# Kernel optimization log

Measured on AMD Instinct MI355X. Metric: run time of the kernel, lower is better.

## Reference

```python
import jax, jax.numpy as jnp
import numpy as np
from math import sqrt

D_K = 64
HEADS = 16


def setup_inputs() -> dict:
    key = jax.random.key(0)
    k1, k2, k3 = jax.random.split(key, 3)
    B, S, D = 2, 2048, HEADS * D_K
    queries = jax.random.normal(k1, (B, S, D), dtype=jnp.float32)
    keys = jax.random.normal(k2, (B, S, D), dtype=jnp.float32)
    values = jax.random.normal(k3, (B, S, D), dtype=jnp.float32)
    # causal mask: 1 where attention is disallowed (j > i), 0 elsewhere
    mask = jnp.triu(jnp.ones((S, S), dtype=jnp.int32), k=1)[None, None]  # [1,1,S,S]
    return {"queries": queries, "keys": keys, "values": values, "mask": mask}


def reference(queries, keys, values, mask):
    B, S, _ = queries.shape
    # [B, S, H*Dk] -> [B, H, S, Dk]
    def split_heads(x):
        return x.reshape(B, -1, HEADS, D_K).transpose(0, 2, 1, 3)

    q = split_heads(queries)
    k = split_heads(keys)
    v = split_heads(values)
    # scores: [B, H, Sq, Sk]
    attn = jnp.einsum('bhqd,bhkd->bhqk', q, k) / sqrt(D_K)
    attn = attn + mask.astype(attn.dtype) * jnp.asarray(-1e9, attn.dtype)
    w = jax.nn.softmax(attn, axis=-1)
    out = jnp.einsum('bhqk,bhkd->bhqd', w, v)  # [B, H, Sq, Dk]
    return out
```

## Files before the change

kernel.cpp:

```cpp
#include <hip/hip_runtime.h>
#include <hip/hip_bf16.h>

#define S_LEN 2048
#define NH 16
#define DK 64
#define DM 1024
#define QBLK 64
#define KVBLK 64
#define NQT 32
#define KPAD 72

typedef float f32x4 __attribute__((ext_vector_type(4)));
typedef __bf16 bf16x8 __attribute__((ext_vector_type(8)));

__device__ __forceinline__ int vswz(int row) { return ((row >> 3) & 3) << 4; }

__device__ __forceinline__ void kv_issue(const float* __restrict__ kp_t,
                                         const float* __restrict__ vp_t,
                                         int tid, int w, int l,
                                         float4 (&kr)[2][2], float (&vr)[16]) {
#pragma unroll
  for (int it = 0; it < 2; ++it) {
    int f = tid + it * 256;
    int row = f >> 3, cb8 = f & 7;
    const float* src = kp_t + (size_t)row * DM + cb8 * 8;
    kr[it][0] = *reinterpret_cast<const float4*>(src);
    kr[it][1] = *reinterpret_cast<const float4*>(src + 4);
  }
#pragma unroll
  for (int it = 0; it < 4; ++it) {
#pragma unroll
    for (int r = 0; r < 4; ++r)
      vr[it * 4 + r] = vp_t[(size_t)(4 * w + 16 * it + r) * DM + l];
  }
}

__device__ __forceinline__ void kv_write(__bf16* __restrict__ Kb, __bf16* __restrict__ Vb,
                                         int tid, int w, int l,
                                         const float4 (&kr)[2][2], const float (&vr)[16]) {
#pragma unroll
  for (int it = 0; it < 2; ++it) {
    int f = tid + it * 256;
    int row = f >> 3, cb8 = f & 7;
    bf16x8 kb;
    kb[0] = (__bf16)kr[it][0].x; kb[1] = (__bf16)kr[it][0].y;
    kb[2] = (__bf16)kr[it][0].z; kb[3] = (__bf16)kr[it][0].w;
    kb[4] = (__bf16)kr[it][1].x; kb[5] = (__bf16)kr[it][1].y;
    kb[6] = (__bf16)kr[it][1].z; kb[7] = (__bf16)kr[it][1].w;
    *reinterpret_cast<bf16x8*>(&Kb[row * KPAD + cb8 * 8]) = kb;
  }
#pragma unroll
  for (int half = 0; half < 2; ++half) {
    bf16x8 vb;
#pragma unroll
    for (int j = 0; j < 8; ++j) vb[j] = (__bf16)vr[half * 8 + j];
    char* p = reinterpret_cast<char*>(Vb) +
              (((l * KPAD + half * 32 + w * 8) * 2) ^ vswz(l));
    *reinterpret_cast<bf16x8*>(p) = vb;
  }
}

__device__ __forceinline__ void mask_diagT(f32x4 (&s)[4], int kv0, int q0,
                                           int w, int l16, int hi) {
  const int ig = q0 + w * 16 + l16;
#pragma unroll
  for (int n = 0; n < 4; ++n)
#pragma unroll
    for (int r = 0; r < 4; ++r) {
      int jg = kv0 + n * 16 + hi * 4 + r;
      if (jg > ig) s[n][r] = -1e30f;
    }
}

__device__ __forceinline__ float sm_expT(f32x4 (&s)[4]) {
  float a0 = 0.f, a1 = 0.f;
#pragma unroll
  for (int n = 0; n < 4; ++n) {
    float p0 = __builtin_amdgcn_exp2f(s[n][0]);
    float p1 = __builtin_amdgcn_exp2f(s[n][1]);
    float p2 = __builtin_amdgcn_exp2f(s[n][2]);
    float p3 = __builtin_amdgcn_exp2f(s[n][3]);
    s[n][0] = p0; s[n][1] = p1; s[n][2] = p2; s[n][3] = p3;
    a0 += p0 + p1;
    a1 += p2 + p3;
  }
  return a0 + a1;
}

__device__ __forceinline__ void packT(const f32x4 (&s)[4], bf16x8 (&pa)[2]) {
#pragma unroll
  for (int c = 0; c < 2; ++c) {
    bf16x8 a;
#pragma unroll
    for (int j = 0; j < 8; ++j) a[j] = (__bf16)s[2 * c + (j >> 2)][j & 3];
    pa[c] = a;
  }
}

__device__ __forceinline__ void load_q_frags(const float* __restrict__ qp, int q0,
                                             int w, int l16, int hi, bf16x8 (&aq)[2]) {
  const float* qr = qp + (size_t)(q0 + w * 16 + l16) * DM;
  const float qs = 0.125f * 1.44269504089f;
#pragma unroll
  for (int c = 0; c < 2; ++c) {
    float4 f0 = *reinterpret_cast<const float4*>(qr + c * 32 + hi * 8);
    float4 f1 = *reinterpret_cast<const float4*>(qr + c * 32 + hi * 8 + 4);
    bf16x8 a;
    a[0] = (__bf16)(f0.x * qs); a[1] = (__bf16)(f0.y * qs);
    a[2] = (__bf16)(f0.z * qs); a[3] = (__bf16)(f0.w * qs);
    a[4] = (__bf16)(f1.x * qs); a[5] = (__bf16)(f1.y * qs);
    a[6] = (__bf16)(f1.z * qs); a[7] = (__bf16)(f1.w * qs);
    aq[c] = a;
  }
}

__device__ __forceinline__ void store_out(float* __restrict__ Og, int b, int h, int q0,
                                          int w, int l, int l16, int hi,
                                          const f32x4 (&o_acc)[4], float l_chain) {
  float lf = l_chain;
  lf += __shfl_xor(lf, 16);
  lf += __shfl_xor(lf, 32);
  float invl = 1.0f / lf;
  float inv[4];
#pragma unroll
  for (int r = 0; r < 4; ++r)
    inv[r] = __shfl(invl, (l & 48) | (hi * 4 + r));
  float* op = Og + ((size_t)(b * NH + h) * S_LEN + q0 + w * 16) * DK;
#pragma unroll
  for (int n = 0; n < 4; ++n)
#pragma unroll
    for (int r = 0; r < 4; ++r)
      op[(size_t)(hi * 4 + r) * DK + n * 16 + l16] = o_acc[n][r] * inv[r];
}

__global__ __launch_bounds__(256, 2)
void fa_fwd_causal(const float* __restrict__ Qg, const float* __restrict__ Kg,
                   const float* __restrict__ Vg, float* __restrict__ Og) {
  __shared__ __align__(16) __bf16 Kl[2][KVBLK * KPAD];
  __shared__ __align__(16) __bf16 Vt[2][DK * KPAD];

  const int bid  = blockIdx.x;
  const int xcd  = bid & 7;
  const int s    = bid >> 3;
  const int p_raw = s & 15;
  const int bb   = (s >> 4) & 1;
  const int hh   = (s >> 5) & 1;
  const int pair = hh ? (15 - p_raw) : p_raw;
  const int b    = bb;
  const int h    = xcd + 8 * hh;

  const int qta = pair;
  const int qtb = NQT - 1 - pair;
  const int q0a = qta * QBLK;
  const int q0b = qtb * QBLK;

  const int tid = threadIdx.x;
  const int w   = tid >> 6;
  const int l   = tid & 63;
  const int l16 = l & 15;
  const int hi  = l >> 4;

  const size_t base_in = (size_t)b * S_LEN * DM + (size_t)h * DK;
  const float* qp = Qg + base_in;
  const float* kp = Kg + base_in;
  const float* vp = Vg + base_in;

  bf16x8 aqA[2], aqB[2];
  load_q_frags(qp, q0a, w, l16, hi, aqA);
  load_q_frags(qp, q0b, w, l16, hi, aqB);

  f32x4 oA[4], oB[4];
  float lA = 0.f, lB = 0.f;
#pragma unroll
  for (int n = 0; n < 4; ++n) { oA[n] = (f32x4){0.f,0.f,0.f,0.f}; oB[n] = (f32x4){0.f,0.f,0.f,0.f}; }

  float4 kr[2][2];
  float  vr[16];
  kv_issue(kp, vp, tid, w, l, kr, vr);

  int cur = 0;
  const int n_tiles = qtb + 1;
  for (int t = 0; t < n_tiles; ++t) {
    const int kv0 = t * KVBLK;
    kv_write(Kl[cur], Vt[cur], tid, w, l, kr, vr);
    if (t + 1 < n_tiles)
      kv_issue(kp + (size_t)(kv0 + KVBLK) * DM, vp + (size_t)(kv0 + KVBLK) * DM,
               tid, w, l, kr, vr);
    __syncthreads();
    const __bf16* Kb = Kl[cur];
    const __bf16* Vb = Vt[cur];

    if (t <= qta) {
      f32x4 sA[4], sB[4];
#pragma unroll
      for (int n = 0; n < 4; ++n) { sA[n] = (f32x4){0.f,0.f,0.f,0.f}; sB[n] = (f32x4){0.f,0.f,0.f,0.f}; }
#pragma unroll
      for (int n = 0; n < 4; ++n)
#pragma unroll
        for (int c = 0; c < 2; ++c) {
          bf16x8 kf = *reinterpret_cast<const bf16x8*>(&Kb[(n * 16 + l16) * KPAD + c * 32 + hi * 8]);
          sB[n] = __builtin_amdgcn_mfma_f32_16x16x32_bf16(kf, aqB[c], sB[n], 0, 0, 0);
          sA[n] = __builtin_amdgcn_mfma_f32_16x16x32_bf16(kf, aqA[c], sA[n], 0, 0, 0);
        }
      if (t == qta) mask_diagT(sA, kv0, q0a, w, l16, hi);
      lB += sm_expT(sB);
      lA += sm_expT(sA);
      bf16x8 paA[2], paB[2];
      packT(sB, paB);
      packT(sA, paA);
#pragma unroll
      for (int c = 0; c < 2; ++c)
#pragma unroll
        for (int n = 0; n < 4; ++n) {
          int row = n * 16 + l16;
          const char* vpb = reinterpret_cast<const char*>(Vb) +
                            (((row * KPAD + c * 32 + hi * 8) * 2) ^ vswz(row));
          bf16x8 vf = *reinterpret_cast<const bf16x8*>(vpb);
          oB[n] = __builtin_amdgcn_mfma_f32_16x16x32_bf16(paB[c], vf, oB[n], 0, 0, 0);
          oA[n] = __builtin_amdgcn_mfma_f32_16x16x32_bf16(paA[c], vf, oA[n], 0, 0, 0);
        }
    } else {
      f32x4 sB[4];
#pragma unroll
      for (int n = 0; n < 4; ++n) sB[n] = (f32x4){0.f,0.f,0.f,0.f};
#pragma unroll
      for (int n = 0; n < 4; ++n)
#pragma unroll
        for (int c = 0; c < 2; ++c) {
          bf16x8 kf = *reinterpret_cast<const bf16x8*>(&Kb[(n * 16 + l16) * KPAD + c * 32 + hi * 8]);
          sB[n] = __builtin_amdgcn_mfma_f32_16x16x32_bf16(kf, aqB[c], sB[n], 0, 0, 0);
        }
      if (t == qtb) mask_diagT(sB, kv0, q0b, w, l16, hi);
      lB += sm_expT(sB);
      bf16x8 paB[2];
      packT(sB, paB);
#pragma unroll
      for (int c = 0; c < 2; ++c)
#pragma unroll
        for (int n = 0; n < 4; ++n) {
          int row = n * 16 + l16;
          const char* vpb = reinterpret_cast<const char*>(Vb) +
                            (((row * KPAD + c * 32 + hi * 8) * 2) ^ vswz(row));
          bf16x8 vf = *reinterpret_cast<const bf16x8*>(vpb);
          oB[n] = __builtin_amdgcn_mfma_f32_16x16x32_bf16(paB[c], vf, oB[n], 0, 0, 0);
        }
    }
    cur ^= 1;
  }

  store_out(Og, b, h, q0a, w, l, l16, hi, oA, lA);
  store_out(Og, b, h, q0b, w, l, l16, hi, oB, lB);
}

extern "C" void kernel_launch(void* const* d_in, const int* in_sizes, int n_in,
                              void* d_out, int out_size, void* d_ws, size_t ws_size,
                              hipStream_t stream) {
  const float* q = (const float*)d_in[0];
  const float* k = (const float*)d_in[1];
  const float* v = (const float*)d_in[2];
  float* out = (float*)d_out;
  const int blocks = 2 * NH * (NQT / 2);
  hipLaunchKernelGGL(fa_fwd_causal, dim3(blocks), dim3(256), 0, stream, q, k, v, out);
}
```

Measured before the change: 43.77 us.

## Split paired causal query tiles into one tile per block, heaviest first

Each block now handles a single 64-row query tile instead of a balanced pair (qt and 31-qt). Blocks are ordered so the longest causal rows launch first, and the grid doubles to 1024 blocks. Launch bounds are raised to 4 blocks per SM, and __syncthreads is replaced by an explicit lgkmcnt wait plus s_barrier. The aim is more occupancy and finer load balancing. The cost is that each K/V tile is now reused by only one query tile, so global K/V loads and conversions roughly double, and register pressure must fit the tighter launch bound.

```diff
diff --git a/kernel.cpp b/kernel.cpp
--- a/kernel.cpp
+++ b/kernel.cpp
@@ -133,26 +133,21 @@
       op[(size_t)(hi * 4 + r) * DK + n * 16 + l16] = o_acc[n][r] * inv[r];
 }
 
-__global__ __launch_bounds__(256, 2)
+__global__ __launch_bounds__(256, 4)
 void fa_fwd_causal(const float* __restrict__ Qg, const float* __restrict__ Kg,
                    const float* __restrict__ Vg, float* __restrict__ Og) {
   __shared__ __align__(16) __bf16 Kl[2][KVBLK * KPAD];
   __shared__ __align__(16) __bf16 Vt[2][DK * KPAD];
 
-  const int bid  = blockIdx.x;
-  const int xcd  = bid & 7;
-  const int s    = bid >> 3;
-  const int p_raw = s & 15;
-  const int bb   = (s >> 4) & 1;
-  const int hh   = (s >> 5) & 1;
-  const int pair = hh ? (15 - p_raw) : p_raw;
-  const int b    = bb;
-  const int h    = xcd + 8 * hh;
-
-  const int qta = pair;
-  const int qtb = NQT - 1 - pair;
-  const int q0a = qta * QBLK;
-  const int q0b = qtb * QBLK;
+  const int bid = blockIdx.x;
+  const int xcd = bid & 7;
+  const int s   = bid >> 3;
+  const int qt  = NQT - 1 - (s & 31);
+  const int hh  = (s >> 5) & 1;
+  const int b   = (s >> 6) & 1;
+  const int h   = xcd + 8 * hh;
+
+  const int q0 = qt * QBLK;
 
   const int tid = threadIdx.x;
   const int w   = tid >> 6;
@@ -165,91 +160,60 @@
   const float* kp = Kg + base_in;
   const float* vp = Vg + base_in;
 
-  bf16x8 aqA[2], aqB[2];
-  load_q_frags(qp, q0a, w, l16, hi, aqA);
-  load_q_frags(qp, q0b, w, l16, hi, aqB);
-
-  f32x4 oA[4], oB[4];
-  float lA = 0.f, lB = 0.f;
-#pragma unroll
-  for (int n = 0; n < 4; ++n) { oA[n] = (f32x4){0.f,0.f,0.f,0.f}; oB[n] = (f32x4){0.f,0.f,0.f,0.f}; }
+  bf16x8 aq[2];
+  load_q_frags(qp, q0, w, l16, hi, aq);
+
+  f32x4 o[4];
+  float lsum = 0.f;
+#pragma unroll
+  for (int n = 0; n < 4; ++n) o[n] = (f32x4){0.f, 0.f, 0.f, 0.f};
 
   float4 kr[2][2];
   float  vr[16];
   kv_issue(kp, vp, tid, w, l, kr, vr);
 
   int cur = 0;
-  const int n_tiles = qtb + 1;
+  const int n_tiles = qt + 1;
   for (int t = 0; t < n_tiles; ++t) {
     const int kv0 = t * KVBLK;
     kv_write(Kl[cur], Vt[cur], tid, w, l, kr, vr);
     if (t + 1 < n_tiles)
       kv_issue(kp + (size_t)(kv0 + KVBLK) * DM, vp + (size_t)(kv0 + KVBLK) * DM,
                tid, w, l, kr, vr);
-    __syncthreads();
+    asm volatile("s_waitcnt lgkmcnt(0)" ::: "memory");
+    __builtin_amdgcn_s_barrier();
+
     const __bf16* Kb = Kl[cur];
     const __bf16* Vb = Vt[cur];
 
-    if (t <= qta) {
-      f32x4 sA[4], sB[4];
-#pragma unroll
-      for (int n = 0; n < 4; ++n) { sA[n] = (f32x4){0.f,0.f,0.f,0.f}; sB[n] = (f32x4){0.f,0.f,0.f,0.f}; }
-#pragma unroll
-      for (int n = 0; n < 4; ++n)
-#pragma unroll
-        for (int c = 0; c < 2; ++c) {
-          bf16x8 kf = *reinterpret_cast<const bf16x8*>(&Kb[(n * 16 + l16) * KPAD + c * 32 + hi * 8]);
-          sB[n] = __builtin_amdgcn_mfma_f32_16x16x32_bf16(kf, aqB[c], sB[n], 0, 0, 0);
-          sA[n] = __builtin_amdgcn_mfma_f32_16x16x32_bf16(kf, aqA[c], sA[n], 0, 0, 0);
-        }
-      if (t == qta) mask_diagT(sA, kv0, q0a, w, l16, hi);
-      lB += sm_expT(sB);
-      lA += sm_expT(sA);
-      bf16x8 paA[2], paB[2];
-      packT(sB, paB);
-      packT(sA, paA);
-#pragma unroll
-      for (int c = 0; c < 2; ++c)
-#pragma unroll
-        for (int n = 0; n < 4; ++n) {
-          int row = n * 16 + l16;
-          const char* vpb = reinterpret_cast<const char*>(Vb) +
-                            (((row * KPAD + c * 32 + hi * 8) * 2) ^ vswz(row));
-          bf16x8 vf = *reinterpret_cast<const bf16x8*>(vpb);
-          oB[n] = __builtin_amdgcn_mfma_f32_16x16x32_bf16(paB[c], vf, oB[n], 0, 0, 0);
-          oA[n] = __builtin_amdgcn_mfma_f32_16x16x32_bf16(paA[c], vf, oA[n], 0, 0, 0);
-        }
-    } else {
-      f32x4 sB[4];
-#pragma unroll
-      for (int n = 0; n < 4; ++n) sB[n] = (f32x4){0.f,0.f,0.f,0.f};
-#pragma unroll
-      for (int n = 0; n < 4; ++n)
-#pragma unroll
-        for (int c = 0; c < 2; ++c) {
-          bf16x8 kf = *reinterpret_cast<const bf16x8*>(&Kb[(n * 16 + l16) * KPAD + c * 32 + hi * 8]);
-          sB[n] = __builtin_amdgcn_mfma_f32_16x16x32_bf16(kf, aqB[c], sB[n], 0, 0, 0);
-        }
-      if (t == qtb) mask_diagT(sB, kv0, q0b, w, l16, hi);
-      lB += sm_expT(sB);
-      bf16x8 paB[2];
-      packT(sB, paB);
-#pragma unroll
-      for (int c = 0; c < 2; ++c)
-#pragma unroll
-        for (int n = 0; n < 4; ++n) {
-          int row = n * 16 + l16;
-          const char* vpb = reinterpret_cast<const char*>(Vb) +
-                            (((row * KPAD + c * 32 + hi * 8) * 2) ^ vswz(row));
-          bf16x8 vf = *reinterpret_cast<const bf16x8*>(vpb);
-          oB[n] = __builtin_amdgcn_mfma_f32_16x16x32_bf16(paB[c], vf, oB[n], 0, 0, 0);
-        }
-    }
+    f32x4 s4[4];
+#pragma unroll
+    for (int n = 0; n < 4; ++n) s4[n] = (f32x4){0.f, 0.f, 0.f, 0.f};
+#pragma unroll
+    for (int n = 0; n < 4; ++n)
+#pragma unroll
+      for (int c = 0; c < 2; ++c) {
+        bf16x8 kf = *reinterpret_cast<const bf16x8*>(&Kb[(n * 16 + l16) * KPAD + c * 32 + hi * 8]);
+        s4[n] = __builtin_amdgcn_mfma_f32_16x16x32_bf16(kf, aq[c], s4[n], 0, 0, 0);
+      }
+    if (t == qt) mask_diagT(s4, kv0, q0, w, l16, hi);
+    lsum += sm_expT(s4);
+    bf16x8 pa[2];
+    packT(s4, pa);
+#pragma unroll
+    for (int c = 0; c < 2; ++c)
+#pragma unroll
+      for (int n = 0; n < 4; ++n) {
+        int row = n * 16 + l16;
+        const char* vpb = reinterpret_cast<const char*>(Vb) +
+                          (((row * KPAD + c * 32 + hi * 8) * 2) ^ vswz(row));
+        bf16x8 vf = *reinterpret_cast<const bf16x8*>(vpb);
+        o[n] = __builtin_amdgcn_mfma_f32_16x16x32_bf16(pa[c], vf, o[n], 0, 0, 0);
+      }
     cur ^= 1;
   }
 
-  store_out(Og, b, h, q0a, w, l, l16, hi, oA, lA);
-  store_out(Og, b, h, q0b, w, l, l16, hi, oB, lB);
+  store_out(Og, b, h, q0, w, l, l16, hi, o, lsum);
 }
 
 extern "C" void kernel_launch(void* const* d_in, const int* in_sizes, int n_in,
@@ -259,6 +223,6 @@
   const float* k = (const float*)d_in[1];
   const float* v = (const float*)d_in[2];
   float* out = (float*)d_out;
-  const int blocks = 2 * NH * (NQT / 2);
+  const int blocks = 2 * NH * NQT;
   hipLaunchKernelGGL(fa_fwd_causal, dim3(blocks), dim3(256), 0, stream, q, k, v, out);
 }
```

Result: slower. 66.69 us (+52.4%).
